# Performance work log

Measured on AMD Instinct MI355X. Metric: run time of the kernel, lower is better.

The kernel has to match this reference:

```python
import jax, jax.numpy as jnp
import numpy as np
import math


def _build_lookup(S):
    # Vectorized port of build_hierarchical_index_lookup_table (static, numpy).
    L = int(math.log2(S))
    total = 2 * S - 1
    max_valid = total - 2  # root is never a neighbor
    idx = np.full((S, L), -1, dtype=np.int32)
    cmask = np.zeros((S, L), dtype=bool)
    n = np.arange(S, dtype=np.int64)
    for lvl in range(L):
        if lvl == 0:
            nn = n ^ 1
            pair = n
        else:
            pair = n // 2 + S
            nn = pair ^ 1
        valid = nn <= max_valid
        idx[:, lvl] = np.where(valid, nn.astype(np.int32), idx[:, lvl])
        cmask[:, lvl] = np.where(valid, (pair < nn) & valid, cmask[:, lvl])
        n = nn
    return jnp.asarray(idx), jnp.asarray(cmask)


def _tree_kv(k, v, levels, scale):
    # Build parent nodes bottom-up. Parent K is the mean of its two children;
    # parent V is refined by the fused parent-self attention (build_parent_nodes):
    # 3-way softmax over [self, child0, child1] with eps 1e-9 in the denominator.
    K_parts, V_parts = [k], [v]
    Kc, Vc = k, v
    for _ in range(levels):
        Kc0, Kc1 = Kc[:, 0::2], Kc[:, 1::2]
        Vc0, Vc1 = Vc[:, 0::2], Vc[:, 1::2]
        Kp = 0.5 * (Kc0 + Kc1)
        Vp = 0.5 * (Vc0 + Vc1)
        s_self = jnp.einsum('bphd,bphd->bph', Kp, Kp) * scale
        s0 = jnp.einsum('bphd,bphd->bph', Kp, Kc0) * scale
        s1 = jnp.einsum('bphd,bphd->bph', Kp, Kc1) * scale
        m = jnp.maximum(s_self, jnp.maximum(s0, s1))
        e_self = jnp.exp(s_self - m)
        e0 = jnp.exp(s0 - m)
        e1 = jnp.exp(s1 - m)
        denom = e_self + e0 + e1 + 1e-9
        Vp = (e_self[..., None] * Vp + e0[..., None] * Vc0 + e1[..., None] * Vc1) / denom[..., None]
        K_parts.append(Kp)
        V_parts.append(Vp)
        Kc, Vc = Kp, Vp
    # Full tree: leaves first, then each parent level -> [B, 2S-1, H, D]
    return jnp.concatenate(K_parts, axis=1), jnp.concatenate(V_parts, axis=1)


def setup_inputs() -> dict:
    key = jax.random.key(0)
    kq, kk, kv = jax.random.split(key, 3)
    B, S, H, D = 4, 4096, 8, 64
    q = jax.random.normal(kq, (B, S, H, D), dtype=jnp.float32)
    k = jax.random.normal(kk, (B, S, H, D), dtype=jnp.float32)
    v = jax.random.normal(kv, (B, S, H, D), dtype=jnp.float32)
    return {'q': q, 'k': k, 'v': v}


def reference(q, k, v):
    B, S, H, D = q.shape
    L = int(math.log2(S))
    scale = 1.0 / math.sqrt(D)
    idx, cmask = _build_lookup(S)          # [S, L] int32, [S, L] bool
    Kf, Vf = _tree_kv(k, v, L, scale)      # [B, 2S-1, H, D]
    kc = Kf[:, idx]                        # [B, S, L, H, D] tree-indexed gather
    vc = Vf[:, idx]
    s_self = jnp.einsum('bshd,bshd->bsh', q, k) * scale
    s_cross = jnp.einsum('bshd,bslhd->bshl', q, kc) * scale
    s_cross = jnp.where(cmask[None, :, None, :], -jnp.inf, s_cross)
    m = jnp.maximum(s_self, jnp.max(s_cross, axis=-1))  # online-softmax max
    e_self = jnp.exp(s_self - m)
    e_cross = jnp.exp(s_cross - m[..., None])
    denom = e_self + jnp.sum(e_cross, axis=-1)
    out = (e_self[..., None] * v + jnp.einsum('bshl,bslhd->bshd', e_cross, vc)) / denom[..., None]
    return out
```

## Files before the change

kernel.cpp:

```cpp
#include <hip/hip_runtime.h>


#define S 4096
#define H 8
#define D 64
#define B 4
#define NBH 32
#define NHI 254
#define SCALE 0.125f
#define ROWF 68

__device__ inline float red16(float x) {
    x += __shfl_xor(x, 1);
    x += __shfl_xor(x, 2);
    x += __shfl_xor(x, 4);
    x += __shfl_xor(x, 8);
    return x;
}

__device__ inline float dot4(const float4 a, const float4 b) {
    return a.x * b.x + a.y * b.y + a.z * b.z + a.w * b.w;
}

__device__ inline void combine(const float4 k0, const float4 k1,
                               const float4 v0, const float4 v1,
                               float4& kp, float4& vp) {
    kp.x = 0.5f * (k0.x + k1.x);
    kp.y = 0.5f * (k0.y + k1.y);
    kp.z = 0.5f * (k0.z + k1.z);
    kp.w = 0.5f * (k0.w + k1.w);
    float pss = red16(dot4(kp, kp)) * SCALE;
    float p0  = red16(dot4(kp, k0)) * SCALE;
    float p1  = red16(dot4(kp, k1)) * SCALE;
    float m  = fmaxf(pss, fmaxf(p0, p1));
    float es = __expf(pss - m), e0 = __expf(p0 - m), e1 = __expf(p1 - m);
    float inv = 1.0f / (es + e0 + e1 + 1e-9f);
    float h = 0.5f * es;
    vp.x = ((h + e0) * v0.x + (h + e1) * v1.x) * inv;
    vp.y = ((h + e0) * v0.y + (h + e1) * v1.y) * inv;
    vp.z = ((h + e0) * v0.z + (h + e1) * v1.z) * inv;
    vp.w = ((h + e0) * v0.w + (h + e1) * v1.w) * inv;
}

__global__ __launch_bounds__(256, 8) void chunk5(
    const float* __restrict__ k, const float* __restrict__ v,
    float* __restrict__ khi, float* __restrict__ vhi)
{
    __shared__ float lsk[32 * ROWF], lsv[32 * ROWF];
    const int t = threadIdx.x;
    const int sub = t & 15;
    const int pg = t >> 4;
    const int blk = blockIdx.x;
    const int pair = blk & 63;
    const int bh = blk >> 6;
    const int b = bh >> 3, h = bh & 7;
    const int csel = pg >> 3;
    const int jg = pg & 7;
    const int c = pair * 2 + csel;
    const int rowBase = csel * 16;

#pragma unroll
    for (int r = 0; r < 2; ++r) {
        int j = jg + r * 8;
        int s0 = c * 32 + 2 * j;
        size_t a0 = ((((size_t)b * S + s0) * H + h) * D) + sub * 4;
        float4 k0 = *(const float4*)(k + a0);
        float4 k1 = *(const float4*)(k + a0 + H * D);
        float4 v0 = *(const float4*)(v + a0);
        float4 v1 = *(const float4*)(v + a0 + H * D);
        float4 kp, vp;
        combine(k0, k1, v0, v1, kp, vp);
        *(float4*)(lsk + (rowBase + j) * ROWF + sub * 4) = kp;
        *(float4*)(lsv + (rowBase + j) * ROWF + sub * 4) = vp;
    }
    __syncthreads();

#pragma unroll
    for (int tt = 1; tt <= 4; ++tt) {
        int nodes = 16 >> tt;
        for (int j = jg; j < nodes; j += 8) {
            int r0 = rowBase + ((2 * j) << (tt - 1));
            int r1 = rowBase + ((2 * j + 1) << (tt - 1));
            float4 k0 = *(const float4*)(lsk + r0 * ROWF + sub * 4);
            float4 k1 = *(const float4*)(lsk + r1 * ROWF + sub * 4);
            float4 v0 = *(const float4*)(lsv + r0 * ROWF + sub * 4);
            float4 v1 = *(const float4*)(lsv + r1 * ROWF + sub * 4);
            float4 kp, vp;
            combine(k0, k1, v0, v1, kp, vp);
            if (tt < 4) {
                *(float4*)(lsk + (rowBase + (j << tt)) * ROWF + sub * 4) = kp;
                *(float4*)(lsv + (rowBase + (j << tt)) * ROWF + sub * 4) = vp;
            } else {
                size_t g = ((size_t)bh * NHI + c) * 64 + sub * 4;
                *(float4*)(khi + g) = kp;
                *(float4*)(vhi + g) = vp;
            }
        }
        __syncthreads();
    }
}

__global__ __launch_bounds__(256) void build_hi_half(
    float* __restrict__ khi, float* __restrict__ vhi)
{
    __shared__ float lk[64 * ROWF], lv[64 * ROWF];
    const int t = threadIdx.x;
    const int sub = t & 15;
    const int pg = t >> 4;
    const int bh = blockIdx.x >> 1;
    const int half = blockIdx.x & 1;
    size_t base = (size_t)bh * NHI * 64;
    const int rootO = half * 64;

    for (int i = t; i < 1024; i += 256) {
        int row = i >> 4, s16 = i & 15;
        *(float4*)(lk + row * ROWF + s16 * 4) =
            *(const float4*)(khi + base + (size_t)(rootO + row) * 64 + s16 * 4);
        *(float4*)(lv + row * ROWF + s16 * 4) =
            *(const float4*)(vhi + base + (size_t)(rootO + row) * 64 + s16 * 4);
    }
    __syncthreads();

#pragma unroll
    for (int tt = 1; tt <= 6; ++tt) {
        int nodes = 64 >> tt;
        int off = 256 - (256 >> tt);
        for (int j = pg; j < nodes; j += 16) {
            int r0 = (2 * j) << (tt - 1);
            int r1 = (2 * j + 1) << (tt - 1);
            float4 k0 = *(const float4*)(lk + r0 * ROWF + sub * 4);
            float4 k1 = *(const float4*)(lk + r1 * ROWF + sub * 4);
            float4 v0 = *(const float4*)(lv + r0 * ROWF + sub * 4);
            float4 v1 = *(const float4*)(lv + r1 * ROWF + sub * 4);
            float4 kp, vp;
            combine(k0, k1, v0, v1, kp, vp);
            *(float4*)(lk + (j << tt) * ROWF + sub * 4) = kp;
            *(float4*)(lv + (j << tt) * ROWF + sub * 4) = vp;
            size_t g = base + (size_t)(off + half * nodes + j) * 64 + sub * 4;
            *(float4*)(khi + g) = kp;
            *(float4*)(vhi + g) = vp;
        }
        __syncthreads();
    }
}

__global__ __launch_bounds__(256, 7) void attn32(
    const float* __restrict__ q, const float* __restrict__ k,
    const float* __restrict__ v,
    const float* __restrict__ khi, const float* __restrict__ vhi,
    float* __restrict__ out)
{
    __shared__ float tk[30 * ROWF], tv[30 * ROWF];
    __shared__ float pk[7 * ROWF], pv[7 * ROWF];
    const int t = threadIdx.x;
    const int sub = t & 15;
    const int pg = t >> 4;
    const int blk = blockIdx.x;
    const int c32 = blk & 127;
    const int bh = blk >> 7;
    const int b = bh >> 3, h = bh & 7;

    {
        int pl = (pg < 7) ? pg : pg - 8;
        if (pl >= 0 && pl < 7 && pg != 7 && pg != 15) {
            if ((c32 >> pl) & 1) {
                int off = 256 - (256 >> pl);
                int node = off + ((c32 >> pl) ^ 1);
                size_t a = ((size_t)bh * NHI + node) * 64 + sub * 4;
                if (pg < 7) *(float4*)(pk + pl * ROWF + sub * 4) = *(const float4*)(khi + a);
                else        *(float4*)(pv + pl * ROWF + sub * 4) = *(const float4*)(vhi + a);
            }
        }
    }

    const int s0 = c32 * 32 + 2 * pg;
    const size_t a0 = ((((size_t)b * S + s0) * H + h) * D) + sub * 4;
    const float4 k0 = *(const float4*)(k + a0);
    const float4 k1 = *(const float4*)(k + a0 + H * D);
    const float4 v0 = *(const float4*)(v + a0);
    const float4 v1 = *(const float4*)(v + a0 + H * D);
    const float4 q0 = *(const float4*)(q + a0);
    const float4 q1 = *(const float4*)(q + a0 + H * D);

    {
        float4 kp, vp;
        combine(k0, k1, v0, v1, kp, vp);
        *(float4*)(tk + pg * ROWF + sub * 4) = kp;
        *(float4*)(tv + pg * ROWF + sub * 4) = vp;
    }
    __syncthreads();

    if (pg < 4) {
#pragma unroll
        for (int u = 0; u < 2; ++u) {
            int j = 2 * pg + u;
            float4 ka = *(const float4*)(tk + (2 * j) * ROWF + sub * 4);
            float4 kb = *(const float4*)(tk + (2 * j + 1) * ROWF + sub * 4);
            float4 va = *(const float4*)(tv + (2 * j) * ROWF + sub * 4);
            float4 vb = *(const float4*)(tv + (2 * j + 1) * ROWF + sub * 4);
            float4 kp, vp;
            combine(ka, kb, va, vb, kp, vp);
            *(float4*)(tk + (16 + j) * ROWF + sub * 4) = kp;
            *(float4*)(tv + (16 + j) * ROWF + sub * 4) = vp;
        }
        {
            float4 ka = *(const float4*)(tk + (16 + 2 * pg) * ROWF + sub * 4);
            float4 kb = *(const float4*)(tk + (16 + 2 * pg + 1) * ROWF + sub * 4);
            float4 va = *(const float4*)(tv + (16 + 2 * pg) * ROWF + sub * 4);
            float4 vb = *(const float4*)(tv + (16 + 2 * pg + 1) * ROWF + sub * 4);
            float4 kp, vp;
            combine(ka, kb, va, vb, kp, vp);
            *(float4*)(tk + (24 + pg) * ROWF + sub * 4) = kp;
            *(float4*)(tv + (24 + pg) * ROWF + sub * 4) = vp;
        }
        if (pg < 2) {
            float4 ka = *(const float4*)(tk + (24 + 2 * pg) * ROWF + sub * 4);
            float4 kb = *(const float4*)(tk + (24 + 2 * pg + 1) * ROWF + sub * 4);
            float4 va = *(const float4*)(tv + (24 + 2 * pg) * ROWF + sub * 4);
            float4 vb = *(const float4*)(tv + (24 + 2 * pg + 1) * ROWF + sub * 4);
            float4 kp, vp;
            combine(ka, kb, va, vb, kp, vp);
            *(float4*)(tk + (28 + pg) * ROWF + sub * 4) = kp;
            *(float4*)(tv + (28 + pg) * ROWF + sub * 4) = vp;
        }
    }
    __syncthreads();

#pragma unroll
    for (int r = 0; r < 2; ++r) {
        const int s = s0 + r;
        const float4 q4 = r ? q1 : q0;
        const float4 k4 = r ? k1 : k0;
        const float4 v4 = r ? v1 : v0;

        float ss = red16(dot4(q4, k4)) * SCALE;

        float sc[12];
        if (r) sc[0] = red16(dot4(q4, k0)) * SCALE;
        else   sc[0] = -1e38f;
#pragma unroll
        for (int l = 1; l <= 4; ++l) {
            if ((s >> l) & 1) {
                int base = 32 - (32 >> (l - 1));
                int loc = base + (((s >> l) ^ 1) - (c32 << (5 - l)));
                float4 kc = *(const float4*)(tk + loc * ROWF + sub * 4);
                sc[l] = red16(dot4(q4, kc)) * SCALE;
            } else sc[l] = -1e38f;
        }
#pragma unroll
        for (int l = 5; l <= 11; ++l) {
            if ((c32 >> (l - 5)) & 1) {
                float4 kc = *(const float4*)(pk + (l - 5) * ROWF + sub * 4);
                sc[l] = red16(dot4(q4, kc)) * SCALE;
            } else sc[l] = -1e38f;
        }

        float m = ss;
#pragma unroll
        for (int l = 0; l < 12; ++l) m = fmaxf(m, sc[l]);

        float es = __expf(ss - m);
        float denom = es;
        float4 acc;
        acc.x = es * v4.x; acc.y = es * v4.y;
        acc.z = es * v4.z; acc.w = es * v4.w;

        if (r) {
            float e = __expf(sc[0] - m);
            denom += e;
            acc.x += e * v0.x; acc.y += e * v0.y;
            acc.z += e * v0.z; acc.w += e * v0.w;
        }
#pragma unroll
        for (int l = 1; l <= 4; ++l) {
            if ((s >> l) & 1) {
                int base = 32 - (32 >> (l - 1));
                int loc = base + (((s >> l) ^ 1) - (c32 << (5 - l)));
                float4 vc = *(const float4*)(tv + loc * ROWF + sub * 4);
                float e = __expf(sc[l] - m);
                denom += e;
                acc.x += e * vc.x; acc.y += e * vc.y;
                acc.z += e * vc.z; acc.w += e * vc.w;
            }
        }
#pragma unroll
        for (int l = 5; l <= 11; ++l) {
            if ((c32 >> (l - 5)) & 1) {
                float4 vc = *(const float4*)(pv + (l - 5) * ROWF + sub * 4);
                float e = __expf(sc[l] - m);
                denom += e;
                acc.x += e * vc.x; acc.y += e * vc.y;
                acc.z += e * vc.z; acc.w += e * vc.w;
            }
        }
        float inv = 1.0f / denom;
        float4 o;
        o.x = acc.x * inv; o.y = acc.y * inv;
        o.z = acc.z * inv; o.w = acc.w * inv;
        *(float4*)(out + a0 + r * H * D) = o;
    }
}

extern "C" void kernel_launch(void* const* d_in, const int* in_sizes, int n_in,
                              void* d_out, int out_size, void* d_ws, size_t ws_size,
                              hipStream_t stream) {
    const float* q = (const float*)d_in[0];
    const float* k = (const float*)d_in[1];
    const float* v = (const float*)d_in[2];
    float* outp = (float*)d_out;
    float* khi = (float*)d_ws;
    float* vhi = khi + (size_t)NBH * NHI * D;

    hipLaunchKernelGGL(chunk5, dim3(NBH * 64), dim3(256), 0, stream,
                       k, v, khi, vhi);
    hipLaunchKernelGGL(build_hi_half, dim3(NBH * 2), dim3(256), 0, stream,
                       khi, vhi);
    hipLaunchKernelGGL(attn32, dim3(NBH * 128), dim3(256), 0, stream,
                       q, k, v, khi, vhi, outp);
}
```

Baseline: 156.8 us.

## Replace LDS tree-reduction levels with wavefront shuffles in chunk and attention kernels

The lower tree levels, both in the chunk builder and in the attention kernel's local subtree build, now combine sibling nodes by exchanging float4 values across lanes with shuffle-xor instead of writing to shared memory and synchronizing between levels. Each thread in chunk5 now loads four leaves and builds two levels in registers. The shared-memory footprint shrinks and most __syncthreads barriers disappear. In exchange the kernels do redundant combine work on paired lanes, more shuffles and higher register pressure, and chunk5's launch-bounds occupancy hint drops from 8 to 6.

```diff
diff --git a/kernel.cpp b/kernel.cpp
--- a/kernel.cpp
+++ b/kernel.cpp
@@ -20,6 +20,24 @@
 
 __device__ inline float dot4(const float4 a, const float4 b) {
     return a.x * b.x + a.y * b.y + a.z * b.z + a.w * b.w;
+}
+
+__device__ inline float4 shfl_xor4(const float4 x, int m) {
+    float4 r;
+    r.x = __shfl_xor(x.x, m);
+    r.y = __shfl_xor(x.y, m);
+    r.z = __shfl_xor(x.z, m);
+    r.w = __shfl_xor(x.w, m);
+    return r;
+}
+
+__device__ inline float4 sel4(bool c, const float4 a, const float4 b) {
+    float4 r;
+    r.x = c ? a.x : b.x;
+    r.y = c ? a.y : b.y;
+    r.z = c ? a.z : b.z;
+    r.w = c ? a.w : b.w;
+    return r;
 }
 
 __device__ inline void combine(const float4 k0, const float4 k1,
@@ -42,11 +60,11 @@
     vp.w = ((h + e0) * v0.w + (h + e1) * v1.w) * inv;
 }
 
-__global__ __launch_bounds__(256, 8) void chunk5(
+__global__ __launch_bounds__(256, 6) void chunk5(
     const float* __restrict__ k, const float* __restrict__ v,
     float* __restrict__ khi, float* __restrict__ vhi)
 {
-    __shared__ float lsk[32 * ROWF], lsv[32 * ROWF];
+    __shared__ float l4k[4 * ROWF], l4v[4 * ROWF];
     const int t = threadIdx.x;
     const int sub = t & 15;
     const int pg = t >> 4;
@@ -57,46 +75,50 @@
     const int csel = pg >> 3;
     const int jg = pg & 7;
     const int c = pair * 2 + csel;
-    const int rowBase = csel * 16;
-
-#pragma unroll
-    for (int r = 0; r < 2; ++r) {
-        int j = jg + r * 8;
-        int s0 = c * 32 + 2 * j;
-        size_t a0 = ((((size_t)b * S + s0) * H + h) * D) + sub * 4;
-        float4 k0 = *(const float4*)(k + a0);
-        float4 k1 = *(const float4*)(k + a0 + H * D);
-        float4 v0 = *(const float4*)(v + a0);
-        float4 v1 = *(const float4*)(v + a0 + H * D);
+
+    const int s0 = c * 32 + 4 * jg;
+    const size_t a0 = ((((size_t)b * S + s0) * H + h) * D) + sub * 4;
+    float4 kA = *(const float4*)(k + a0);
+    float4 kB = *(const float4*)(k + a0 + H * D);
+    float4 kC = *(const float4*)(k + a0 + 2 * H * D);
+    float4 kD = *(const float4*)(k + a0 + 3 * H * D);
+    float4 vA = *(const float4*)(v + a0);
+    float4 vB = *(const float4*)(v + a0 + H * D);
+    float4 vC = *(const float4*)(v + a0 + 2 * H * D);
+    float4 vD = *(const float4*)(v + a0 + 3 * H * D);
+
+    float4 k1a, v1a, k1b, v1b, k2, v2;
+    combine(kA, kB, vA, vB, k1a, v1a);
+    combine(kC, kD, vC, vD, k1b, v1b);
+    combine(k1a, k1b, v1a, v1b, k2, v2);
+
+    float4 p2k = shfl_xor4(k2, 16), p2v = shfl_xor4(v2, 16);
+    float4 k3, v3;
+    combine(sel4(jg & 1, p2k, k2), sel4(jg & 1, k2, p2k),
+            sel4(jg & 1, p2v, v2), sel4(jg & 1, v2, p2v), k3, v3);
+
+    float4 p3k = shfl_xor4(k3, 32), p3v = shfl_xor4(v3, 32);
+    float4 k4, v4;
+    combine(sel4(jg & 2, p3k, k3), sel4(jg & 2, k3, p3k),
+            sel4(jg & 2, p3v, v3), sel4(jg & 2, v3, p3v), k4, v4);
+
+    if ((jg & 3) == 0) {
+        int row = csel * 2 + (jg >> 2);
+        *(float4*)(l4k + row * ROWF + sub * 4) = k4;
+        *(float4*)(l4v + row * ROWF + sub * 4) = v4;
+    }
+    __syncthreads();
+    if (jg == 0) {
+        int r0 = csel * 2, r1 = csel * 2 + 1;
+        float4 ka4 = *(const float4*)(l4k + r0 * ROWF + sub * 4);
+        float4 kb4 = *(const float4*)(l4k + r1 * ROWF + sub * 4);
+        float4 va4 = *(const float4*)(l4v + r0 * ROWF + sub * 4);
+        float4 vb4 = *(const float4*)(l4v + r1 * ROWF + sub * 4);
         float4 kp, vp;
-        combine(k0, k1, v0, v1, kp, vp);
-        *(float4*)(lsk + (rowBase + j) * ROWF + sub * 4) = kp;
-        *(float4*)(lsv + (rowBase + j) * ROWF + sub * 4) = vp;
-    }
-    __syncthreads();
-
-#pragma unroll
-    for (int tt = 1; tt <= 4; ++tt) {
-        int nodes = 16 >> tt;
-        for (int j = jg; j < nodes; j += 8) {
-            int r0 = rowBase + ((2 * j) << (tt - 1));
-            int r1 = rowBase + ((2 * j + 1) << (tt - 1));
-            float4 k0 = *(const float4*)(lsk + r0 * ROWF + sub * 4);
-            float4 k1 = *(const float4*)(lsk + r1 * ROWF + sub * 4);
-            float4 v0 = *(const float4*)(lsv + r0 * ROWF + sub * 4);
-            float4 v1 = *(const float4*)(lsv + r1 * ROWF + sub * 4);
-            float4 kp, vp;
-            combine(k0, k1, v0, v1, kp, vp);
-            if (tt < 4) {
-                *(float4*)(lsk + (rowBase + (j << tt)) * ROWF + sub * 4) = kp;
-                *(float4*)(lsv + (rowBase + (j << tt)) * ROWF + sub * 4) = vp;
-            } else {
-                size_t g = ((size_t)bh * NHI + c) * 64 + sub * 4;
-                *(float4*)(khi + g) = kp;
-                *(float4*)(vhi + g) = vp;
-            }
-        }
-        __syncthreads();
+        combine(ka4, kb4, va4, vb4, kp, vp);
+        size_t g = ((size_t)bh * NHI + c) * 64 + sub * 4;
+        *(float4*)(khi + g) = kp;
+        *(float4*)(vhi + g) = vp;
     }
 }
 
@@ -182,47 +204,39 @@
     const float4 q0 = *(const float4*)(q + a0);
     const float4 q1 = *(const float4*)(q + a0 + H * D);
 
-    {
+    float4 t1k, t1v;
+    combine(k0, k1, v0, v1, t1k, t1v);
+    *(float4*)(tk + pg * ROWF + sub * 4) = t1k;
+    *(float4*)(tv + pg * ROWF + sub * 4) = t1v;
+
+    float4 p2k = shfl_xor4(t1k, 16), p2v = shfl_xor4(t1v, 16);
+    float4 t2k, t2v;
+    combine(sel4(pg & 1, p2k, t1k), sel4(pg & 1, t1k, p2k),
+            sel4(pg & 1, p2v, t1v), sel4(pg & 1, t1v, p2v), t2k, t2v);
+    if ((pg & 1) == 0) {
+        *(float4*)(tk + (16 + (pg >> 1)) * ROWF + sub * 4) = t2k;
+        *(float4*)(tv + (16 + (pg >> 1)) * ROWF + sub * 4) = t2v;
+    }
+
+    float4 p3k = shfl_xor4(t2k, 32), p3v = shfl_xor4(t2v, 32);
+    float4 t3k, t3v;
+    combine(sel4(pg & 2, p3k, t2k), sel4(pg & 2, t2k, p3k),
+            sel4(pg & 2, p3v, t2v), sel4(pg & 2, t2v, p3v), t3k, t3v);
+    if ((pg & 3) == 0) {
+        *(float4*)(tk + (24 + (pg >> 2)) * ROWF + sub * 4) = t3k;
+        *(float4*)(tv + (24 + (pg >> 2)) * ROWF + sub * 4) = t3v;
+    }
+    __syncthreads();
+
+    if (pg < 2) {
+        float4 ka = *(const float4*)(tk + (24 + 2 * pg) * ROWF + sub * 4);
+        float4 kb = *(const float4*)(tk + (24 + 2 * pg + 1) * ROWF + sub * 4);
+        float4 va = *(const float4*)(tv + (24 + 2 * pg) * ROWF + sub * 4);
+        float4 vb = *(const float4*)(tv + (24 + 2 * pg + 1) * ROWF + sub * 4);
         float4 kp, vp;
-        combine(k0, k1, v0, v1, kp, vp);
-        *(float4*)(tk + pg * ROWF + sub * 4) = kp;
-        *(float4*)(tv + pg * ROWF + sub * 4) = vp;
-    }
-    __syncthreads();
-
-    if (pg < 4) {
-#pragma unroll
-        for (int u = 0; u < 2; ++u) {
-            int j = 2 * pg + u;
-            float4 ka = *(const float4*)(tk + (2 * j) * ROWF + sub * 4);
-            float4 kb = *(const float4*)(tk + (2 * j + 1) * ROWF + sub * 4);
-            float4 va = *(const float4*)(tv + (2 * j) * ROWF + sub * 4);
-            float4 vb = *(const float4*)(tv + (2 * j + 1) * ROWF + sub * 4);
-            float4 kp, vp;
-            combine(ka, kb, va, vb, kp, vp);
-            *(float4*)(tk + (16 + j) * ROWF + sub * 4) = kp;
-            *(float4*)(tv + (16 + j) * ROWF + sub * 4) = vp;
-        }
-        {
-            float4 ka = *(const float4*)(tk + (16 + 2 * pg) * ROWF + sub * 4);
-            float4 kb = *(const float4*)(tk + (16 + 2 * pg + 1) * ROWF + sub * 4);
-            float4 va = *(const float4*)(tv + (16 + 2 * pg) * ROWF + sub * 4);
-            float4 vb = *(const float4*)(tv + (16 + 2 * pg + 1) * ROWF + sub * 4);
-            float4 kp, vp;
-            combine(ka, kb, va, vb, kp, vp);
-            *(float4*)(tk + (24 + pg) * ROWF + sub * 4) = kp;
-            *(float4*)(tv + (24 + pg) * ROWF + sub * 4) = vp;
-        }
-        if (pg < 2) {
-            float4 ka = *(const float4*)(tk + (24 + 2 * pg) * ROWF + sub * 4);
-            float4 kb = *(const float4*)(tk + (24 + 2 * pg + 1) * ROWF + sub * 4);
-            float4 va = *(const float4*)(tv + (24 + 2 * pg) * ROWF + sub * 4);
-            float4 vb = *(const float4*)(tv + (24 + 2 * pg + 1) * ROWF + sub * 4);
-            float4 kp, vp;
-            combine(ka, kb, va, vb, kp, vp);
-            *(float4*)(tk + (28 + pg) * ROWF + sub * 4) = kp;
-            *(float4*)(tv + (28 + pg) * ROWF + sub * 4) = vp;
-        }
+        combine(ka, kb, va, vb, kp, vp);
+        *(float4*)(tk + (28 + pg) * ROWF + sub * 4) = kp;
+        *(float4*)(tv + (28 + pg) * ROWF + sub * 4) = vp;
     }
     __syncthreads();
 
```

Result: slower. 161.8 us (+3.2%).
